# Kernel tuning notes

Measured on AMD Instinct MI355X. Metric: run time of the kernel, lower is better.

## Reference

```python
import jax, jax.numpy as jnp
import numpy as np

N = 100000   # num_nodes
E = 1600000  # num_edges (avg degree 16)
D = 64       # embed_channels
C = 16       # num_classes
EPSILON = 0.1  # AntiSymmetricConv step size (PyG default)
GAMMA = 0.1    # AntiSymmetricConv diffusion strength (PyG default)


def setup_inputs() -> dict:
    key = jax.random.key(0)
    ks = jax.random.split(key, 9)
    s = 1.0 / np.sqrt(D)
    return {
        "edge_index": jax.random.randint(ks[0], (2, E), 0, N, dtype=jnp.int32),
        "embed_w": jax.random.normal(ks[1], (N, D), dtype=jnp.float32) * 0.1,
        "W_rel": jax.random.normal(ks[2], (D, D), dtype=jnp.float32) * s,   # GraphConv lin_rel weight
        "b_rel": jax.random.normal(ks[3], (D,), dtype=jnp.float32) * s,     # GraphConv lin_rel bias
        "W_root": jax.random.normal(ks[4], (D, D), dtype=jnp.float32) * s,  # GraphConv lin_root weight (no bias)
        "W_anti": jax.random.normal(ks[5], (D, D), dtype=jnp.float32) * s,  # AntiSymmetricConv W
        "b_anti": jax.random.normal(ks[6], (D,), dtype=jnp.float32) * s,    # AntiSymmetricConv bias
        "W_lin": jax.random.normal(ks[7], (C, D), dtype=jnp.float32) * s,   # lin2 weight
        "b_lin": jax.random.normal(ks[8], (C,), dtype=jnp.float32) * s,     # lin2 bias
    }


def reference(edge_index, embed_w, W_rel, b_rel, W_root, W_anti, b_anti, W_lin, b_lin):
    x = embed_w  # [N, D] node features = embedding table
    src, dst = edge_index[0], edge_index[1]
    # phi = GraphConv with 'add' aggregation: lin_rel(sum_j x_j) + lin_root(x)
    agg = jax.ops.segment_sum(x[src], dst, num_segments=N)  # [N, D] sparse gather+scatter-add
    h = agg @ W_rel.T + b_rel + x @ W_root.T
    # antisymmetric weight: W - W^T - gamma * I
    aW = W_anti - W_anti.T - GAMMA * jnp.eye(D, dtype=x.dtype)
    h = x @ aW.T + h + b_anti
    h = jnp.tanh(h)                       # default act of AntiSymmetricConv
    x = x + EPSILON * h                   # single iteration (num_iters=1 default)
    # dropout p=0.0 -> identity
    out = jax.nn.sigmoid(x @ W_lin.T + b_lin)  # [N, C]
    return out
```

## Files before the change

kernel.cpp:

```cpp
#include <hip/hip_runtime.h>

#define DD 64
#define CC 16
#define EPSILON 0.1f
#define GAMMA 0.1f
#define BSH 6
#define BSZ 64
#define CAP 1280
#define MAXBK 2048
#define PAD 68
#define PADW 65
#define CSH 10
#define MAXNC 128
#define NREP 8
#define SEGC 2560
#define CPAD 16
#define CAPC 20480
#define L1CHUNK 2048
#define L1THR 512
#define NSLICE 8

typedef float v2f __attribute__((ext_vector_type(2)));
typedef __attribute__((ext_vector_type(8))) short short8v;
typedef __attribute__((ext_vector_type(4))) float f32x4;

static __device__ inline short f2bf(float f) {
    unsigned u = __builtin_bit_cast(unsigned, f);
    unsigned r = (u + 0x7FFFu + ((u >> 16) & 1u)) >> 16;
    return (short)r;
}

__global__ __launch_bounds__(L1THR) void bin_coarse_conv(
        const int* __restrict__ ei, int* __restrict__ gcntc,
        unsigned* __restrict__ binned_c, int E,
        const float* __restrict__ x, unsigned* __restrict__ x_q, int N,
        const float* __restrict__ Wrel, const float* __restrict__ Wroot,
        const float* __restrict__ Wanti, const float* __restrict__ brel,
        const float* __restrict__ banti,
        unsigned short* __restrict__ Bp, float* __restrict__ bc) {
    __shared__ int hist[MAXNC], gbase[MAXNC], cur[MAXNC];
    const int t = threadIdx.x;
    const int rep = blockIdx.x & (NREP - 1);
    if (t < MAXNC) { hist[t] = 0; cur[t] = 0; }
    __syncthreads();
    const int e0 = blockIdx.x * L1CHUNK;
    int srcv[4], dstv[4];
    const int e = e0 + 4 * t;
    if (e + 4 <= E) {
        int4 s4 = *(const int4*)&ei[e];
        int4 d4 = *(const int4*)&ei[E + e];
        srcv[0] = s4.x; srcv[1] = s4.y; srcv[2] = s4.z; srcv[3] = s4.w;
        dstv[0] = d4.x; dstv[1] = d4.y; dstv[2] = d4.z; dstv[3] = d4.w;
    } else {
#pragma unroll
        for (int i = 0; i < 4; ++i) {
            if (e + i < E) { srcv[i] = ei[e + i]; dstv[i] = ei[E + e + i]; }
            else dstv[i] = -1;
        }
    }
#pragma unroll
    for (int i = 0; i < 4; ++i)
        if (dstv[i] >= 0) atomicAdd(&hist[dstv[i] >> CSH], 1);
    __syncthreads();
    if (t < MAXNC) {
        int h = hist[t];
        gbase[t] = h ? atomicAdd(&gcntc[(t * NREP + rep) * CPAD], h) : 0;
    }
    __syncthreads();
#pragma unroll
    for (int i = 0; i < 4; ++i) {
        if (dstv[i] >= 0) {
            int b = dstv[i] >> CSH;
            int pos = gbase[b] + atomicAdd(&cur[b], 1);
            if (pos < SEGC)
                binned_c[(size_t)b * CAPC + rep * SEGC + pos] =
                    (unsigned)srcv[i] |
                    ((unsigned)(dstv[i] & ((1 << CSH) - 1)) << 17);
        }
    }
    if (blockIdx.x == 0) {
        for (int idx = t; idx < 16 * 64 * 8; idx += L1THR) {
            int j = idx & 7, l = (idx >> 3) & 63;
            int nt = (idx >> 9) & 3, ks = idx >> 11;
            int k = ks * 32 + ((l >> 4) << 3) + j;
            int d = nt * 16 + (l & 15);
            float v;
            if (k < 64) {
                v = Wrel[d * 64 + k];
            } else {
                int j2 = k - 64;
                v = Wroot[d * 64 + j2] + Wanti[d * 64 + j2] - Wanti[j2 * 64 + d];
                if (d == j2) v -= GAMMA;
            }
            Bp[idx] = (unsigned short)f2bf(v);
        }
        if (t < 64) bc[t] = brel[t] + banti[t];
    }
    const float4* x4 = (const float4*)x;
    const int M = N * (DD / 4);
    const int G = gridDim.x * L1THR;
    for (int i = blockIdx.x * L1THR + t; i < M; i += G) {
        float4 a = x4[i];
        int r = __builtin_amdgcn_cvt_pk_fp8_f32(a.x, a.y, 0, false);
        r = __builtin_amdgcn_cvt_pk_fp8_f32(a.z, a.w, r, true);
        x_q[i] = (unsigned)r;
    }
}

__global__ __launch_bounds__(256) void bin_fine(
        const int* __restrict__ gcntc, const unsigned* __restrict__ binned_c,
        int* __restrict__ gcnt, unsigned* __restrict__ binned) {
    __shared__ int hist[16];
    __shared__ int hbase[16];
    const int t = threadIdx.x;
    const int c = blockIdx.x >> 3, s = blockIdx.x & (NSLICE - 1);
    int cnt = gcntc[(c * NREP + s) * CPAD];
    if (cnt > SEGC) cnt = SEGC;
    if (t < 16) hist[t] = 0;
    __syncthreads();
    const unsigned* bcp = binned_c + (size_t)c * CAPC + s * SEGC;
    unsigned ent[10];
#pragma unroll
    for (int j = 0; j < 10; ++j) {
        int i = t + j * 256;
        ent[j] = (i < cnt) ? bcp[i] : 0xFFFFFFFFu;
        if (ent[j] != 0xFFFFFFFFu) atomicAdd(&hist[ent[j] >> (17 + BSH)], 1);
    }
    __syncthreads();
    if (t < 16) {
        hbase[t] = hist[t] ? atomicAdd(&gcnt[c * 16 + t], hist[t]) : 0;
        hist[t] = 0;
    }
    __syncthreads();
#pragma unroll
    for (int j = 0; j < 10; ++j) {
        if (ent[j] != 0xFFFFFFFFu) {
            unsigned dstc = ent[j] >> 17;
            int f = dstc >> BSH;
            int pos = hbase[f] + atomicAdd(&hist[f], 1);
            if (pos < CAP)
                binned[(size_t)(c * 16 + f) * CAP + pos] =
                    (ent[j] & 0x1FFFF) | ((dstc & (BSZ - 1)) << 17);
        }
    }
}

__global__ __launch_bounds__(512, 6) void mega(
        const float* __restrict__ x, const unsigned* __restrict__ x_q,
        const int* __restrict__ gcnt, const unsigned* __restrict__ binned,
        const unsigned short* __restrict__ Bp, const float* __restrict__ bc,
        const float* __restrict__ Wlin, const float* __restrict__ blin,
        float* __restrict__ out, int N) {
    __shared__ float R0[BSZ * PAD];
    __shared__ float wl_sh[CC * PADW];
    __shared__ int csr[CAP];
    __shared__ int deg[BSZ], offs[BSZ], cur[BSZ];

    const int t = threadIdx.x;
    const int b = blockIdx.x;
    const int nb0 = b << BSH;
    int cnt = gcnt[b];
    if (cnt > CAP) cnt = CAP;
    const unsigned* bl = binned + (size_t)b * CAP;

#pragma unroll
    for (int i = 0; i < 2; ++i) {
        int idx = t + 512 * i;
        wl_sh[(idx >> 6) * PADW + (idx & 63)] = Wlin[idx];
    }
    if (t < BSZ) deg[t] = 0;
    __syncthreads();
    for (int i = t; i < cnt; i += 512) atomicAdd(&deg[bl[i] >> 17], 1);
    __syncthreads();
    if (t < 64) {
        int v = deg[t];
#pragma unroll
        for (int off = 1; off < 64; off <<= 1) {
            int u = __shfl_up(v, off, 64);
            if (t >= off) v += u;
        }
        offs[t] = v - deg[t];
        cur[t] = v - deg[t];
    }
    __syncthreads();
    for (int i = t; i < cnt; i += 512) {
        unsigned en = bl[i];
        int pos = atomicAdd(&cur[en >> 17], 1);
        csr[pos] = (int)(en & 0x1FFFF);
    }
    __syncthreads();

    {
        const int g = t >> 3, q = t & 7;
        const uint2* xq2 = (const uint2*)x_q;
        const int i0 = offs[g], dc = deg[g];
        float a[8];
#pragma unroll
        for (int r = 0; r < 8; ++r) a[r] = 0.f;
        int i = 0;
        for (; i + 8 <= dc; i += 8) {
            int s0 = csr[i0 + i + 0], s1 = csr[i0 + i + 1];
            int s2 = csr[i0 + i + 2], s3 = csr[i0 + i + 3];
            int s4 = csr[i0 + i + 4], s5 = csr[i0 + i + 5];
            int s6 = csr[i0 + i + 6], s7 = csr[i0 + i + 7];
            uint2 v0 = xq2[s0 * 8 + q];
            uint2 v1 = xq2[s1 * 8 + q];
            uint2 v2 = xq2[s2 * 8 + q];
            uint2 v3 = xq2[s3 * 8 + q];
            uint2 v4 = xq2[s4 * 8 + q];
            uint2 v5 = xq2[s5 * 8 + q];
            uint2 v6 = xq2[s6 * 8 + q];
            uint2 v7 = xq2[s7 * 8 + q];
            v2f f;
#define ACC8(v)                                                               \
            f = __builtin_amdgcn_cvt_pk_f32_fp8((v).x, false); a[0] += f.x; a[1] += f.y; \
            f = __builtin_amdgcn_cvt_pk_f32_fp8((v).x, true);  a[2] += f.x; a[3] += f.y; \
            f = __builtin_amdgcn_cvt_pk_f32_fp8((v).y, false); a[4] += f.x; a[5] += f.y; \
            f = __builtin_amdgcn_cvt_pk_f32_fp8((v).y, true);  a[6] += f.x; a[7] += f.y;
            ACC8(v0); ACC8(v1); ACC8(v2); ACC8(v3);
            ACC8(v4); ACC8(v5); ACC8(v6); ACC8(v7);
        }
        for (; i < dc; ++i) {
            int s0 = csr[i0 + i];
            uint2 v0 = xq2[s0 * 8 + q];
            v2f f;
            ACC8(v0);
#undef ACC8
        }
        float* row = &R0[g * PAD + 8 * q];
#pragma unroll
        for (int r = 0; r < 8; ++r) row[r] = a[r];
    }
    __syncthreads();

    const int lane = t & 63;
    const int w = t >> 6;
    const int nt = w & 3, mbase = (w >> 2) * 32;
    const int arow = (mbase + (lane & 15)) * PAD + ((lane >> 4) << 3);
    f32x4 acc0 = {0.f, 0.f, 0.f, 0.f}, acc1 = {0.f, 0.f, 0.f, 0.f};

#define LDFRAG(dst, p) do {                                                   \
        float4 u_ = *(const float4*)(p);                                      \
        float4 v_ = *(const float4*)((p) + 4);                                \
        dst[0] = f2bf(u_.x); dst[1] = f2bf(u_.y);                             \
        dst[2] = f2bf(u_.z); dst[3] = f2bf(u_.w);                             \
        dst[4] = f2bf(v_.x); dst[5] = f2bf(v_.y);                             \
        dst[6] = f2bf(v_.z); dst[7] = f2bf(v_.w);                             \
    } while (0)

    {
        short8v b0 = *(const short8v*)&Bp[((0 * 4 + nt) * 64 + lane) * 8];
        short8v b1 = *(const short8v*)&Bp[((1 * 4 + nt) * 64 + lane) * 8];
        short8v a00, a01, a10, a11;
        LDFRAG(a00, &R0[arow]);
        LDFRAG(a01, &R0[arow + 32]);
        LDFRAG(a10, &R0[arow + 16 * PAD]);
        LDFRAG(a11, &R0[arow + 16 * PAD + 32]);
        acc0 = __builtin_amdgcn_mfma_f32_16x16x32_bf16(a00, b0, acc0, 0, 0, 0);
        acc1 = __builtin_amdgcn_mfma_f32_16x16x32_bf16(a10, b0, acc1, 0, 0, 0);
        acc0 = __builtin_amdgcn_mfma_f32_16x16x32_bf16(a01, b1, acc0, 0, 0, 0);
        acc1 = __builtin_amdgcn_mfma_f32_16x16x32_bf16(a11, b1, acc1, 0, 0, 0);
    }
    __syncthreads();

    {
        int nn = N - nb0;
        if (nn > BSZ) nn = BSZ;
        const float4* x4 = (const float4*)x;
        for (int idx = t; idx < nn * 16; idx += 512) {
            float4 v = x4[nb0 * 16 + idx];
            float* row = &R0[(idx >> 4) * PAD + (idx & 15) * 4];
            row[0] = v.x; row[1] = v.y; row[2] = v.z; row[3] = v.w;
        }
    }
    __syncthreads();

    {
        short8v b2 = *(const short8v*)&Bp[((2 * 4 + nt) * 64 + lane) * 8];
        short8v b3 = *(const short8v*)&Bp[((3 * 4 + nt) * 64 + lane) * 8];
        short8v a00, a01, a10, a11;
        LDFRAG(a00, &R0[arow]);
        LDFRAG(a01, &R0[arow + 32]);
        LDFRAG(a10, &R0[arow + 16 * PAD]);
        LDFRAG(a11, &R0[arow + 16 * PAD + 32]);
        acc0 = __builtin_amdgcn_mfma_f32_16x16x32_bf16(a00, b2, acc0, 0, 0, 0);
        acc1 = __builtin_amdgcn_mfma_f32_16x16x32_bf16(a10, b2, acc1, 0, 0, 0);
        acc0 = __builtin_amdgcn_mfma_f32_16x16x32_bf16(a01, b3, acc0, 0, 0, 0);
        acc1 = __builtin_amdgcn_mfma_f32_16x16x32_bf16(a11, b3, acc1, 0, 0, 0);
    }
#undef LDFRAG
    __syncthreads();

    {
        const int dcol = nt * 16 + (lane & 15);
        const float bcv = bc[dcol];
#pragma unroll
        for (int mt = 0; mt < 2; ++mt) {
            f32x4 A = mt ? acc1 : acc0;
#pragma unroll
            for (int r = 0; r < 4; ++r) {
                int nloc = mbase + mt * 16 + ((lane >> 4) << 2) + r;
                float h = A[r] + bcv;
                float e2 = __expf(2.0f * h);
                float th = 1.0f - 2.0f / (e2 + 1.0f);
                float xv = R0[nloc * PAD + dcol];
                R0[nloc * PAD + dcol] = xv + EPSILON * th;
            }
        }
    }
    __syncthreads();

    {
        const int g = t >> 3, q = t & 7;
        const int n = nb0 + g;
        if (n < N) {
            float p0 = blin[2 * q], p1 = blin[2 * q + 1];
#pragma unroll 8
            for (int d = 0; d < DD; ++d) {
                float xv = R0[g * PAD + d];
                p0 = fmaf(xv, wl_sh[(2 * q) * PADW + d], p0);
                p1 = fmaf(xv, wl_sh[(2 * q + 1) * PADW + d], p1);
            }
            float2 o;
            o.x = 1.0f / (1.0f + __expf(-p0));
            o.y = 1.0f / (1.0f + __expf(-p1));
            *(float2*)(out + (size_t)n * CC + 2 * q) = o;
        }
    }
}

extern "C" void kernel_launch(void* const* d_in, const int* in_sizes, int n_in,
                              void* d_out, int out_size, void* d_ws, size_t ws_size,
                              hipStream_t stream) {
    const int*   ei    = (const int*)d_in[0];
    const float* x     = (const float*)d_in[1];
    const float* Wrel  = (const float*)d_in[2];
    const float* brel  = (const float*)d_in[3];
    const float* Wroot = (const float*)d_in[4];
    const float* Wanti = (const float*)d_in[5];
    const float* banti = (const float*)d_in[6];
    const float* Wlin  = (const float*)d_in[7];
    const float* blin  = (const float*)d_in[8];
    float* out = (float*)d_out;

    const int E = in_sizes[0] / 2;
    const int N = in_sizes[1] / DD;
    const int NC = (N + (1 << CSH) - 1) >> CSH;

    unsigned* x_q = (unsigned*)d_ws;
    unsigned* binned_c = x_q + (size_t)N * (DD / 4);
    unsigned* binned = binned_c + (size_t)MAXNC * CAPC;
    int*   gcntc = (int*)(binned + (size_t)MAXBK * CAP);
    int*   gcnt  = gcntc + MAXNC * NREP * CPAD;
    unsigned short* Bp = (unsigned short*)(gcnt + MAXBK);
    float* bc    = (float*)(Bp + 16 * 64 * 8);

    hipMemsetAsync(gcntc, 0, (MAXNC * NREP * CPAD + MAXBK) * sizeof(int), stream);
    bin_coarse_conv<<<(E + L1CHUNK - 1) / L1CHUNK, L1THR, 0, stream>>>(
        ei, gcntc, binned_c, E, x, x_q, N,
        Wrel, Wroot, Wanti, brel, banti, Bp, bc);
    bin_fine<<<NC * NSLICE, 256, 0, stream>>>(gcntc, binned_c, gcnt, binned);
    mega<<<NC * 16, 512, 0, stream>>>(x, x_q, gcnt, binned, Bp, bc, Wlin, blin,
                                      out, N);
}
```

Before: 151.3 us.

## Replace two-level edge binning with single-pass fine binning into replicated segments

Drops the coarse-then-fine two-kernel binning. A single kernel now histograms each edge chunk of 8192 edges directly into 2048 fine buckets of 64 destination nodes, writing to 8 replicated per-bucket segments of 192 slots. The mega kernel reads the 8 segments per block instead of one contiguous bin. This removes one kernel launch and a full extra pass over the binned edges, in exchange for larger shared histograms, more global atomics per block and more scattered writes. Edges past a segment's 192-slot capacity are silently dropped under skewed degree.

```diff
diff --git a/kernel.cpp b/kernel.cpp
--- a/kernel.cpp
+++ b/kernel.cpp
@@ -7,18 +7,13 @@
 #define BSH 6
 #define BSZ 64
 #define CAP 1280
-#define MAXBK 2048
+#define NFB 2048
+#define NREP 8
+#define SEGF 192
 #define PAD 68
 #define PADW 65
-#define CSH 10
-#define MAXNC 128
-#define NREP 8
-#define SEGC 2560
-#define CPAD 16
-#define CAPC 20480
-#define L1CHUNK 2048
-#define L1THR 512
-#define NSLICE 8
+#define FCHUNK 8192
+#define FTHR 512
 
 typedef float v2f __attribute__((ext_vector_type(2)));
 typedef __attribute__((ext_vector_type(8))) short short8v;
@@ -30,56 +25,62 @@
     return (short)r;
 }
 
-__global__ __launch_bounds__(L1THR) void bin_coarse_conv(
-        const int* __restrict__ ei, int* __restrict__ gcntc,
-        unsigned* __restrict__ binned_c, int E,
+__global__ __launch_bounds__(FTHR) void bin_conv(
+        const int* __restrict__ ei, int* __restrict__ gcnt,
+        unsigned* __restrict__ binned, int E,
         const float* __restrict__ x, unsigned* __restrict__ x_q, int N,
         const float* __restrict__ Wrel, const float* __restrict__ Wroot,
         const float* __restrict__ Wanti, const float* __restrict__ brel,
         const float* __restrict__ banti,
         unsigned short* __restrict__ Bp, float* __restrict__ bc) {
-    __shared__ int hist[MAXNC], gbase[MAXNC], cur[MAXNC];
+    __shared__ int hist[NFB], gbase[NFB], cur[NFB];
     const int t = threadIdx.x;
     const int rep = blockIdx.x & (NREP - 1);
-    if (t < MAXNC) { hist[t] = 0; cur[t] = 0; }
-    __syncthreads();
-    const int e0 = blockIdx.x * L1CHUNK;
-    int srcv[4], dstv[4];
-    const int e = e0 + 4 * t;
-    if (e + 4 <= E) {
-        int4 s4 = *(const int4*)&ei[e];
-        int4 d4 = *(const int4*)&ei[E + e];
-        srcv[0] = s4.x; srcv[1] = s4.y; srcv[2] = s4.z; srcv[3] = s4.w;
-        dstv[0] = d4.x; dstv[1] = d4.y; dstv[2] = d4.z; dstv[3] = d4.w;
-    } else {
-#pragma unroll
-        for (int i = 0; i < 4; ++i) {
-            if (e + i < E) { srcv[i] = ei[e + i]; dstv[i] = ei[E + e + i]; }
-            else dstv[i] = -1;
-        }
-    }
-#pragma unroll
-    for (int i = 0; i < 4; ++i)
-        if (dstv[i] >= 0) atomicAdd(&hist[dstv[i] >> CSH], 1);
-    __syncthreads();
-    if (t < MAXNC) {
-        int h = hist[t];
-        gbase[t] = h ? atomicAdd(&gcntc[(t * NREP + rep) * CPAD], h) : 0;
-    }
-    __syncthreads();
-#pragma unroll
-    for (int i = 0; i < 4; ++i) {
+    for (int i = t; i < NFB; i += FTHR) { hist[i] = 0; cur[i] = 0; }
+    __syncthreads();
+    const int e0 = blockIdx.x * FCHUNK;
+    int srcv[16], dstv[16];
+#pragma unroll
+    for (int jj = 0; jj < 4; ++jj) {
+        int e4 = e0 + 4 * (t + FTHR * jj);
+        if (e4 + 4 <= E) {
+            int4 s4 = *(const int4*)&ei[e4];
+            int4 d4 = *(const int4*)&ei[E + e4];
+            srcv[4 * jj + 0] = s4.x; srcv[4 * jj + 1] = s4.y;
+            srcv[4 * jj + 2] = s4.z; srcv[4 * jj + 3] = s4.w;
+            dstv[4 * jj + 0] = d4.x; dstv[4 * jj + 1] = d4.y;
+            dstv[4 * jj + 2] = d4.z; dstv[4 * jj + 3] = d4.w;
+        } else {
+#pragma unroll
+            for (int i = 0; i < 4; ++i) {
+                int e = e4 + i;
+                if (e < E) { srcv[4 * jj + i] = ei[e]; dstv[4 * jj + i] = ei[E + e]; }
+                else dstv[4 * jj + i] = -1;
+            }
+        }
+    }
+#pragma unroll
+    for (int i = 0; i < 16; ++i)
+        if (dstv[i] >= 0) atomicAdd(&hist[dstv[i] >> BSH], 1);
+    __syncthreads();
+    for (int i = t; i < NFB; i += FTHR) {
+        int h = hist[i];
+        gbase[i] = h ? atomicAdd(&gcnt[i * NREP + rep], h) : 0;
+    }
+    __syncthreads();
+#pragma unroll
+    for (int i = 0; i < 16; ++i) {
         if (dstv[i] >= 0) {
-            int b = dstv[i] >> CSH;
-            int pos = gbase[b] + atomicAdd(&cur[b], 1);
-            if (pos < SEGC)
-                binned_c[(size_t)b * CAPC + rep * SEGC + pos] =
+            int fb = dstv[i] >> BSH;
+            int pos = gbase[fb] + atomicAdd(&cur[fb], 1);
+            if (pos < SEGF)
+                binned[((size_t)fb * NREP + rep) * SEGF + pos] =
                     (unsigned)srcv[i] |
-                    ((unsigned)(dstv[i] & ((1 << CSH) - 1)) << 17);
+                    ((unsigned)(dstv[i] & (BSZ - 1)) << 17);
         }
     }
     if (blockIdx.x == 0) {
-        for (int idx = t; idx < 16 * 64 * 8; idx += L1THR) {
+        for (int idx = t; idx < 16 * 64 * 8; idx += FTHR) {
             int j = idx & 7, l = (idx >> 3) & 63;
             int nt = (idx >> 9) & 3, ks = idx >> 11;
             int k = ks * 32 + ((l >> 4) << 3) + j;
@@ -98,50 +99,12 @@
     }
     const float4* x4 = (const float4*)x;
     const int M = N * (DD / 4);
-    const int G = gridDim.x * L1THR;
-    for (int i = blockIdx.x * L1THR + t; i < M; i += G) {
+    const int G = gridDim.x * FTHR;
+    for (int i = blockIdx.x * FTHR + t; i < M; i += G) {
         float4 a = x4[i];
         int r = __builtin_amdgcn_cvt_pk_fp8_f32(a.x, a.y, 0, false);
         r = __builtin_amdgcn_cvt_pk_fp8_f32(a.z, a.w, r, true);
         x_q[i] = (unsigned)r;
-    }
-}
-
-__global__ __launch_bounds__(256) void bin_fine(
-        const int* __restrict__ gcntc, const unsigned* __restrict__ binned_c,
-        int* __restrict__ gcnt, unsigned* __restrict__ binned) {
-    __shared__ int hist[16];
-    __shared__ int hbase[16];
-    const int t = threadIdx.x;
-    const int c = blockIdx.x >> 3, s = blockIdx.x & (NSLICE - 1);
-    int cnt = gcntc[(c * NREP + s) * CPAD];
-    if (cnt > SEGC) cnt = SEGC;
-    if (t < 16) hist[t] = 0;
-    __syncthreads();
-    const unsigned* bcp = binned_c + (size_t)c * CAPC + s * SEGC;
-    unsigned ent[10];
-#pragma unroll
-    for (int j = 0; j < 10; ++j) {
-        int i = t + j * 256;
-        ent[j] = (i < cnt) ? bcp[i] : 0xFFFFFFFFu;
-        if (ent[j] != 0xFFFFFFFFu) atomicAdd(&hist[ent[j] >> (17 + BSH)], 1);
-    }
-    __syncthreads();
-    if (t < 16) {
-        hbase[t] = hist[t] ? atomicAdd(&gcnt[c * 16 + t], hist[t]) : 0;
-        hist[t] = 0;
-    }
-    __syncthreads();
-#pragma unroll
-    for (int j = 0; j < 10; ++j) {
-        if (ent[j] != 0xFFFFFFFFu) {
-            unsigned dstc = ent[j] >> 17;
-            int f = dstc >> BSH;
-            int pos = hbase[f] + atomicAdd(&hist[f], 1);
-            if (pos < CAP)
-                binned[(size_t)(c * 16 + f) * CAP + pos] =
-                    (ent[j] & 0x1FFFF) | ((dstc & (BSZ - 1)) << 17);
-        }
     }
 }
 
@@ -159,9 +122,20 @@
     const int t = threadIdx.x;
     const int b = blockIdx.x;
     const int nb0 = b << BSH;
-    int cnt = gcnt[b];
-    if (cnt > CAP) cnt = CAP;
-    const unsigned* bl = binned + (size_t)b * CAP;
+    const unsigned* segbase = binned + (size_t)b * NREP * SEGF;
+
+    int cnt_r[NREP];
+    {
+        int total = 0;
+#pragma unroll
+        for (int r = 0; r < NREP; ++r) {
+            int c = gcnt[b * NREP + r];
+            if (c > SEGF) c = SEGF;
+            if (total + c > CAP) c = CAP - total;
+            cnt_r[r] = c;
+            total += c;
+        }
+    }
 
 #pragma unroll
     for (int i = 0; i < 2; ++i) {
@@ -170,7 +144,12 @@
     }
     if (t < BSZ) deg[t] = 0;
     __syncthreads();
-    for (int i = t; i < cnt; i += 512) atomicAdd(&deg[bl[i] >> 17], 1);
+#pragma unroll
+    for (int r = 0; r < NREP; ++r) {
+        const unsigned* seg = segbase + r * SEGF;
+        for (int i = t; i < cnt_r[r]; i += 512)
+            atomicAdd(&deg[seg[i] >> 17], 1);
+    }
     __syncthreads();
     if (t < 64) {
         int v = deg[t];
@@ -183,10 +162,14 @@
         cur[t] = v - deg[t];
     }
     __syncthreads();
-    for (int i = t; i < cnt; i += 512) {
-        unsigned en = bl[i];
-        int pos = atomicAdd(&cur[en >> 17], 1);
-        csr[pos] = (int)(en & 0x1FFFF);
+#pragma unroll
+    for (int r = 0; r < NREP; ++r) {
+        const unsigned* seg = segbase + r * SEGF;
+        for (int i = t; i < cnt_r[r]; i += 512) {
+            unsigned en = seg[i];
+            int pos = atomicAdd(&cur[en >> 17], 1);
+            csr[pos] = (int)(en & 0x1FFFF);
+        }
     }
     __syncthreads();
 
@@ -345,21 +328,18 @@
 
     const int E = in_sizes[0] / 2;
     const int N = in_sizes[1] / DD;
-    const int NC = (N + (1 << CSH) - 1) >> CSH;
+    const int NB = (N + BSZ - 1) / BSZ;
 
     unsigned* x_q = (unsigned*)d_ws;
-    unsigned* binned_c = x_q + (size_t)N * (DD / 4);
-    unsigned* binned = binned_c + (size_t)MAXNC * CAPC;
-    int*   gcntc = (int*)(binned + (size_t)MAXBK * CAP);
-    int*   gcnt  = gcntc + MAXNC * NREP * CPAD;
-    unsigned short* Bp = (unsigned short*)(gcnt + MAXBK);
+    unsigned* binned = x_q + (size_t)N * (DD / 4);
+    int*   gcnt  = (int*)(binned + (size_t)NFB * NREP * SEGF);
+    unsigned short* Bp = (unsigned short*)(gcnt + NFB * NREP);
     float* bc    = (float*)(Bp + 16 * 64 * 8);
 
-    hipMemsetAsync(gcntc, 0, (MAXNC * NREP * CPAD + MAXBK) * sizeof(int), stream);
-    bin_coarse_conv<<<(E + L1CHUNK - 1) / L1CHUNK, L1THR, 0, stream>>>(
-        ei, gcntc, binned_c, E, x, x_q, N,
+    hipMemsetAsync(gcnt, 0, NFB * NREP * sizeof(int), stream);
+    bin_conv<<<(E + FCHUNK - 1) / FCHUNK, FTHR, 0, stream>>>(
+        ei, gcnt, binned, E, x, x_q, N,
         Wrel, Wroot, Wanti, brel, banti, Bp, bc);
-    bin_fine<<<NC * NSLICE, 256, 0, stream>>>(gcntc, binned_c, gcnt, binned);
-    mega<<<NC * 16, 512, 0, stream>>>(x, x_q, gcnt, binned, Bp, bc, Wlin, blin,
-                                      out, N);
+    mega<<<NB, 512, 0, stream>>>(x, x_q, gcnt, binned, Bp, bc, Wlin, blin,
+                                 out, N);
 }
```

Measured after the change: 158.6 us. +4.8%, slower.
